# Kernel optimization log

Measured on AMD Instinct MI355X. Metric: run time of the kernel, lower is better.

Reference implementation:

```python
import jax, jax.numpy as jnp
import numpy as np

WIN = (7, 7)          # window_size (M, M)
DIM = 128             # C
HEADS = 4
B = 64                # images
NW = 64               # windows per image
NG = WIN[0] * WIN[1]  # 49 tokens per window
NT = 3136             # total patches per image (56x56)


def _relative_position_index(wh, ww):
    # Faithful to the TF code (default 'xy' meshgrid ordering, global token at (0,0))
    coords = np.stack(np.meshgrid(np.arange(wh), np.arange(ww)))        # (2, ww, wh)
    flat = coords.reshape(2, wh * ww)                                    # (2, M^2)
    flat1 = np.concatenate([flat, np.array([[0], [0]])], axis=1)         # (2, M^2+1)
    rel = flat[:, :, None] - flat1[:, None, :]                           # (2, M^2, M^2+1)
    rel = rel.transpose(1, 2, 0).astype(np.int32)
    rel[:, :, 0] += wh - 1
    rel[:, :, 1] += ww - 1
    rel[:, :, 0] *= 2 * ww - 1
    return rel.sum(-1)                                                   # (M^2, M^2+1)


def setup_inputs() -> dict:
    key = jax.random.key(0)
    ks = jax.random.split(key, 9)
    C, H = DIM, HEADS
    B_ = B * NW
    table_sz = (2 * WIN[0] - 1) * (2 * WIN[1] - 1)  # 169
    return {
        "x": jax.random.normal(ks[0], (B_, NG, C), jnp.float32),
        "xtotal": jax.random.normal(ks[1], (B, NT, C), jnp.float32),
        "xavg": jax.random.normal(ks[2], (B, 1, C), jnp.float32),
        "mask": jnp.zeros((NW, NG, NG + 1), jnp.float32),
        "W_q": jax.random.normal(ks[3], (C, C), jnp.float32) * (C ** -0.5),
        "b_q": jax.random.normal(ks[4], (C,), jnp.float32) * 0.02,
        "W_kv": jax.random.normal(ks[5], (C, 2 * C), jnp.float32) * (C ** -0.5),
        "b_kv": jax.random.normal(ks[6], (2 * C,), jnp.float32) * 0.02,
        "bias_table": jax.random.normal(ks[7], (table_sz, H), jnp.float32) * 0.02,
        "rel_idx": jnp.asarray(_relative_position_index(*WIN), jnp.int32),
    }


def reference(x, xtotal, xavg, mask, W_q, b_q, W_kv, b_kv, bias_table, rel_idx):
    B_, NGl, C = x.shape
    Bl = xavg.shape[0]
    H = bias_table.shape[1]
    d = C // H
    scale = d ** -0.5
    N = NGl + 1

    # window path: concat repeated global token, project kv / q
    xavgR = jnp.repeat(xavg, B_ // Bl, axis=0)               # (B_, 1, C)
    x_c = jnp.concatenate([x, xavgR], axis=1)                # (B_, N, C)
    kv = (x_c @ W_kv + b_kv).reshape(B_, N, 2, H, d).transpose(2, 0, 3, 1, 4)
    k, v = kv[0], kv[1]                                      # (B_, H, N, d)
    q = ((x @ W_q + b_q).reshape(B_, NGl, H, d).transpose(0, 2, 1, 3)) * scale

    attn = jnp.einsum('bhnd,bhmd->bhnm', q, k)               # (B_, H, NG, N)
    bias = bias_table[rel_idx.reshape(-1)].reshape(NGl, N, H).transpose(2, 0, 1)
    attn = attn + bias[None]
    nW = mask.shape[0]
    attn = attn.reshape(B_ // nW, nW, H, NGl, N) + mask[None, :, None]
    attn = jax.nn.softmax(attn.reshape(B_, H, NGl, N), axis=-1)
    x_out = jnp.einsum('bhnm,bhmd->bhnd', attn, v).transpose(0, 2, 1, 3).reshape(B_, NGl, C)

    # global path: q_avg (NOT scaled in the original), attends over all patches
    Nt = xtotal.shape[1]
    kvg = (xtotal @ W_kv + b_kv).reshape(Bl, Nt, 2, H, d).transpose(2, 0, 3, 1, 4)
    kg, vg = kvg[0], kvg[1]                                  # (B, H, Nt, d)
    q_avg = (xavg @ W_q + b_q).reshape(Bl, 1, H, d).transpose(0, 2, 1, 3)
    attng = jax.nn.softmax(jnp.einsum('bhqd,bhmd->bhqm', q_avg, kg), axis=-1)
    xavg_out = jnp.einsum('bhqm,bhmd->bhqd', attng, vg).transpose(0, 2, 1, 3).reshape(Bl, 1, C)
    return x_out, xavg_out
```

## Files before the change

kernel.cpp:

```cpp
#include <hip/hip_runtime.h>
#include <hip/hip_bf16.h>

#define NB_  4096
#define NG_  49
#define NC_  128
#define NH_  4
#define DH_  32
#define NN_  50
#define NIMG 64
#define NT_  3136
#define SCALE_ 0.17677669529663687f

#define WT_LO_OFF 49152
#define BM_OFF    98304
#define SBUF_F    573440

typedef unsigned short u16;
typedef unsigned int   u32;
typedef __attribute__((ext_vector_type(8))) short bf16x8;
typedef __attribute__((ext_vector_type(4))) float f32x4;

__device__ __forceinline__ float b2f(u16 u) {
    union { u32 i; float f; } v; v.i = ((u32)u) << 16; return v.f;
}
__device__ __forceinline__ u16 f2b(float f) {
    union { float f; u32 i; } v; v.f = f;
    u32 x = v.i;
    return (u16)((x + 0x7fffu + ((x >> 16) & 1u)) >> 16);
}
__device__ __forceinline__ u32 pk2(float a, float b) {
    union { __hip_bfloat162 h2; u32 u; } v;
    v.h2 = __float22bfloat162_rn(make_float2(a, b));
    return v.u;
}

extern "C" __global__ __launch_bounds__(256)
void prep_kernel(const float* __restrict__ Wq, const float* __restrict__ Wkv,
                 const float* __restrict__ btab, const int* __restrict__ ridx,
                 const float* __restrict__ mask, u16* __restrict__ ws)
{
    __shared__ int   ridxS[NG_ * NN_];
    __shared__ float btabS[169 * NH_];
    const int t = threadIdx.x, b = blockIdx.x;
    if (b < 24) {
        const int tn = b, kt = t >> 6, lane = t & 63;
        const int j  = tn * 16 + (lane & 15);
        const int k0 = kt * 32 + (lane >> 4) * 8;
        const float qs = (j < 128) ? SCALE_ : 1.f;
        u32 hi[4], lo[4];
        #pragma unroll
        for (int p = 0; p < 4; ++p) {
            const int k = k0 + 2 * p;
            float w0 = ((j < 128) ? Wq[(size_t)k * 128 + j]       : Wkv[(size_t)k * 256 + (j - 128)]) * qs;
            float w1 = ((j < 128) ? Wq[(size_t)(k + 1) * 128 + j] : Wkv[(size_t)(k + 1) * 256 + (j - 128)]) * qs;
            u16 h0 = f2b(w0), h1 = f2b(w1);
            hi[p] = (u32)h0 | ((u32)h1 << 16);
            lo[p] = (u32)f2b(w0 - b2f(h0)) | ((u32)f2b(w1 - b2f(h1)) << 16);
        }
        const size_t fo = ((size_t)(tn * 4 + kt) * 64 + lane) * 8;
        *(uint4*)(ws + fo)             = make_uint4(hi[0], hi[1], hi[2], hi[3]);
        *(uint4*)(ws + WT_LO_OFF + fo) = make_uint4(lo[0], lo[1], lo[2], lo[3]);
    } else {
        const int wx = b - 24;
        for (int i = t; i < NG_ * NN_; i += 256) ridxS[i] = ridx[i];
        for (int i = t; i < 169 * NH_; i += 256) btabS[i] = btab[i];
        __syncthreads();
        for (int i = t; i < NH_ * 16 * 64; i += 256) {
            const int lane = i & 63, tile = (i >> 6) & 15, h = i >> 10;
            const int n  = 16 * (tile >> 2) + (lane & 15);
            const int m0 = 16 * (tile & 3) + 4 * (lane >> 4);
            u16 vv[4];
            #pragma unroll
            for (int e = 0; e < 4; ++e) {
                const int m = m0 + e;
                float val = -1e30f;
                if (n < NG_ && m < NN_)
                    val = btabS[ridxS[n * NN_ + m] * NH_ + h] + mask[((size_t)wx * NG_ + n) * NN_ + m];
                vv[e] = f2b(val);
            }
            u32* dst = (u32*)(ws + BM_OFF + ((size_t)((wx * NH_ + h) * 16 + tile) * 64 + lane) * 4);
            dst[0] = (u32)vv[0] | ((u32)vv[1] << 16);
            dst[1] = (u32)vv[2] | ((u32)vv[3] << 16);
        }
    }
}

struct WinShared {
    u16 q[64][128];
    u16 k[64][128];
    u16 buf[64 * 128];
};
struct GlobShared {
    float qa[NH_][DH_];
    float xavgS[NC_];
    float u[NH_][NC_];
    float cst[NH_];
    float smax[NH_];
    float ssum[NH_];
    float red[256];
    float wpart[2][NH_][NC_];
};
union SMem { WinShared w; GlobShared g; };

extern "C" __global__ __launch_bounds__(256, 4)
void wa2_kernel(const float* __restrict__ x, const float* __restrict__ xtotal,
                const float* __restrict__ xavg,
                const float* __restrict__ Wq, const float* __restrict__ bq,
                const float* __restrict__ Wkv, const float* __restrict__ bkv,
                float* __restrict__ out, u16* __restrict__ ws)
{
    __shared__ SMem sm;
    const int t = threadIdx.x;
    const int blk = blockIdx.x;

    if (blk >= NIMG) {
        WinShared& S = sm.w;
        const int wb   = blk - NIMG;
        const int img  = wb >> 6;
        const int widx = wb & 63;
        const int lane = t & 63, wv = t >> 6;
        const int l15  = lane & 15, g = lane >> 4;

        {
            u16* xc = S.buf;
            const float2* xr = (const float2*)(x + (size_t)wb * (NG_ * NC_));
            for (int i = t; i < NG_ * 64; i += 256) {
                const int row = i >> 6, cp = i & 63;
                float2 xv = xr[i];
                *(u32*)&xc[row * 128 + ((2 * cp) ^ ((row & 7) << 3))] = pk2(xv.x, xv.y);
            }
            if (t < 64) {
                float2 av = ((const float2*)(xavg + (size_t)img * NC_))[t];
                *(u32*)&xc[49 * 128 + ((2 * t) ^ 8)] = pk2(av.x, av.y);
            }
            for (int i = t; i < 14 * 64; i += 256) {
                const int row = 50 + (i >> 6), cp = i & 63;
                *(u32*)&xc[row * 128 + ((2 * cp) ^ ((row & 7) << 3))] = 0u;
            }
        }
        __syncthreads();

        const int sw = (l15 & 7) << 3;

        bf16x8 a[4][4];
        #pragma unroll
        for (int tm = 0; tm < 4; ++tm)
            #pragma unroll
            for (int kt = 0; kt < 4; ++kt)
                a[tm][kt] = *(const bf16x8*)&S.buf[(16 * tm + l15) * 128 + ((32 * kt + 8 * g) ^ sw)];
        __syncthreads();

        {
            u16* vT = S.buf;
            for (int i = 0; i < 6; ++i) {
                const int tn = 6 * wv + i;
                const int jc = tn * 16 + l15;
                const float bias = (jc < 128) ? bq[jc] * SCALE_ : bkv[jc - 128];
                f32x4 acc[4];
                #pragma unroll
                for (int tm = 0; tm < 4; ++tm) acc[tm] = (f32x4){bias, bias, bias, bias};
                #pragma unroll
                for (int kt = 0; kt < 4; ++kt) {
                    const size_t fo = ((size_t)(tn * 4 + kt) * 64 + lane) * 8;
                    bf16x8 bh = *(const bf16x8*)(ws + fo);
                    bf16x8 bl = *(const bf16x8*)(ws + WT_LO_OFF + fo);
                    #pragma unroll
                    for (int tm = 0; tm < 4; ++tm) {
                        acc[tm] = __builtin_amdgcn_mfma_f32_16x16x32_bf16(a[tm][kt], bh, acc[tm], 0, 0, 0);
                        acc[tm] = __builtin_amdgcn_mfma_f32_16x16x32_bf16(a[tm][kt], bl, acc[tm], 0, 0, 0);
                    }
                }
                #pragma unroll
                for (int tm = 0; tm < 4; ++tm) {
                    #pragma unroll
                    for (int rp = 0; rp < 2; ++rp) {
                        const int r0 = 16 * tm + 4 * g + 2 * rp;
                        const u32 p = pk2(acc[tm][2 * rp], acc[tm][2 * rp + 1]);
                        if (jc < 128) {
                            S.q[r0][jc ^ ((r0 & 7) << 3)]           = (u16)p;
                            S.q[r0 + 1][jc ^ (((r0 + 1) & 7) << 3)] = (u16)(p >> 16);
                        } else if (jc < 256) {
                            const int c = jc - 128;
                            S.k[r0][c ^ ((r0 & 7) << 3)]           = (u16)p;
                            S.k[r0 + 1][c ^ (((r0 + 1) & 7) << 3)] = (u16)(p >> 16);
                        } else {
                            const int c = jc - 256, swc = (c & 7) << 3;
                            vT[c * 64 + (r0 ^ swc)]       = (u16)p;
                            vT[c * 64 + ((r0 + 1) ^ swc)] = (u16)(p >> 16);
                        }
                    }
                }
            }
        }
        __syncthreads();

        {
            const int h = wv;
            const u16* vT = S.buf;
            bf16x8 ka[4], qb[4];
            #pragma unroll
            for (int tk = 0; tk < 4; ++tk)
                ka[tk] = *(const bf16x8*)&S.k[16 * tk + l15][(32 * h + 8 * g) ^ sw];
            #pragma unroll
            for (int tq = 0; tq < 4; ++tq)
                qb[tq] = *(const bf16x8*)&S.q[16 * tq + l15][(32 * h + 8 * g) ^ sw];

            const u16* bmb = ws + BM_OFF + (size_t)(widx * NH_ + h) * 4096;
            f32x4 s[4][4];
            #pragma unroll
            for (int tq = 0; tq < 4; ++tq)
                #pragma unroll
                for (int tk = 0; tk < 4; ++tk) {
                    uint2 bm = *(const uint2*)(bmb + ((size_t)(tq * 4 + tk) * 64 + lane) * 4);
                    f32x4 c0;
                    c0[0] = b2f((u16)bm.x); c0[1] = b2f((u16)(bm.x >> 16));
                    c0[2] = b2f((u16)bm.y); c0[3] = b2f((u16)(bm.y >> 16));
                    s[tk][tq] = __builtin_amdgcn_mfma_f32_16x16x32_bf16(ka[tk], qb[tq], c0, 0, 0, 0);
                }

            float inv[4];
            #pragma unroll
            for (int tq = 0; tq < 4; ++tq) {
                float m = s[0][tq][0];
                #pragma unroll
                for (int tk = 0; tk < 4; ++tk)
                    #pragma unroll
                    for (int r = 0; r < 4; ++r) m = fmaxf(m, s[tk][tq][r]);
                m = fmaxf(m, __shfl_xor(m, 16));
                m = fmaxf(m, __shfl_xor(m, 32));
                float sum = 0.f;
                #pragma unroll
                for (int tk = 0; tk < 4; ++tk)
                    #pragma unroll
                    for (int r = 0; r < 4; ++r) {
                        float e = __expf(s[tk][tq][r] - m);
                        s[tk][tq][r] = e;
                        sum += e;
                    }
                sum += __shfl_xor(sum, 16);
                sum += __shfl_xor(sum, 32);
                inv[tq] = 1.f / sum;
            }

            bf16x8 pa[4][2];
            #pragma unroll
            for (int tq = 0; tq < 4; ++tq) {
                const float iv = inv[tq];
                #pragma unroll
                for (int kt = 0; kt < 2; ++kt) {
                    union { u32 u[4]; bf16x8 v; } P;
                    P.u[0] = pk2(s[2 * kt][tq][0] * iv, s[2 * kt][tq][1] * iv);
                    P.u[1] = pk2(s[2 * kt][tq][2] * iv, s[2 * kt][tq][3] * iv);
                    P.u[2] = pk2(s[2 * kt + 1][tq][0] * iv, s[2 * kt + 1][tq][1] * iv);
                    P.u[3] = pk2(s[2 * kt + 1][tq][2] * iv, s[2 * kt + 1][tq][3] * iv);
                    pa[tq][kt] = P.v;
                }
            }
            bf16x8 vb[2][2];
            #pragma unroll
            for (int tn = 0; tn < 2; ++tn) {
                const int c = 32 * h + 16 * tn + l15;
                const int swv = (c & 7) << 3;
                #pragma unroll
                for (int kt = 0; kt < 2; ++kt) {
                    union { uint2 u2[2]; bf16x8 v; } B;
                    B.u2[0] = *(const uint2*)&vT[c * 64 + ((32 * kt + 4 * g) ^ swv)];
                    B.u2[1] = *(const uint2*)&vT[c * 64 + ((32 * kt + 16 + 4 * g) ^ swv)];
                    vb[kt][tn] = B.v;
                }
            }
            #pragma unroll
            for (int tq = 0; tq < 4; ++tq)
                #pragma unroll
                for (int tn = 0; tn < 2; ++tn) {
                    f32x4 acc = {0.f, 0.f, 0.f, 0.f};
                    acc = __builtin_amdgcn_mfma_f32_16x16x32_bf16(pa[tq][0], vb[0][tn], acc, 0, 0, 0);
                    acc = __builtin_amdgcn_mfma_f32_16x16x32_bf16(pa[tq][1], vb[1][tn], acc, 0, 0, 0);
                    #pragma unroll
                    for (int r = 0; r < 4; ++r) {
                        const int row = 16 * tq + 4 * g + r;
                        if (row < NG_)
                            out[(size_t)wb * (NG_ * NC_) + (size_t)row * NC_ + 32 * h + 16 * tn + l15] = acc[r];
                    }
                }
        }
    } else {
        GlobShared& S = sm.g;
        const int img = blk;
        float* sb = (float*)ws + SBUF_F + (size_t)img * (NT_ * NH_);

        if (t < NC_) S.xavgS[t] = xavg[img * NC_ + t];
        __syncthreads();

        if (t < NC_) {
            const int h = t >> 5, jj = t & 31;
            float acc = bq[h * DH_ + jj];
            for (int c = 0; c < NC_; ++c) acc += S.xavgS[c] * Wq[c * NC_ + h * DH_ + jj];
            S.qa[h][jj] = acc;
        }
        __syncthreads();

        if (t < NC_) {
            const int c = t;
            #pragma unroll
            for (int h = 0; h < NH_; ++h) {
                float acc = 0.f;
                const float* wr = Wkv + (size_t)c * (2 * NC_) + h * DH_;
                #pragma unroll
                for (int jj = 0; jj < DH_; ++jj) acc += wr[jj] * S.qa[h][jj];
                S.u[h][c] = acc;
            }
        } else if (t < NC_ + NH_) {
            const int h = t - NC_;
            float acc = 0.f;
            for (int jj = 0; jj < DH_; ++jj) acc += S.qa[h][jj] * bkv[h * DH_ + jj];
            S.cst[h] = acc;
        }
        __syncthreads();

        float lmax0 = -1e30f, lmax1 = -1e30f, lmax2 = -1e30f, lmax3 = -1e30f;
        for (int m = t; m < NT_; m += 256) {
            const float* xr = xtotal + (size_t)(img * NT_ + m) * NC_;
            float a0 = S.cst[0], a1 = S.cst[1], a2 = S.cst[2], a3 = S.cst[3];
            for (int c = 0; c < NC_; ++c) {
                float xv = xr[c];
                a0 += xv * S.u[0][c];
                a1 += xv * S.u[1][c];
                a2 += xv * S.u[2][c];
                a3 += xv * S.u[3][c];
            }
            *(float4*)&sb[m * NH_] = make_float4(a0, a1, a2, a3);
            lmax0 = fmaxf(lmax0, a0); lmax1 = fmaxf(lmax1, a1);
            lmax2 = fmaxf(lmax2, a2); lmax3 = fmaxf(lmax3, a3);
        }
        float lm[NH_] = {lmax0, lmax1, lmax2, lmax3};
        for (int h = 0; h < NH_; ++h) {
            __syncthreads();
            S.red[t] = lm[h];
            __syncthreads();
            for (int off = 128; off > 0; off >>= 1) {
                if (t < off) S.red[t] = fmaxf(S.red[t], S.red[t + off]);
                __syncthreads();
            }
            if (t == 0) S.smax[h] = S.red[0];
        }
        __syncthreads();

        float ls[NH_] = {0.f, 0.f, 0.f, 0.f};
        for (int m = t; m < NT_; m += 256) {
            float4 sv = *(const float4*)&sb[m * NH_];
            sv.x = __expf(sv.x - S.smax[0]); ls[0] += sv.x;
            sv.y = __expf(sv.y - S.smax[1]); ls[1] += sv.y;
            sv.z = __expf(sv.z - S.smax[2]); ls[2] += sv.z;
            sv.w = __expf(sv.w - S.smax[3]); ls[3] += sv.w;
            *(float4*)&sb[m * NH_] = sv;
        }
        for (int h = 0; h < NH_; ++h) {
            __syncthreads();
            S.red[t] = ls[h];
            __syncthreads();
            for (int off = 128; off > 0; off >>= 1) {
                if (t < off) S.red[t] += S.red[t + off];
                __syncthreads();
            }
            if (t == 0) S.ssum[h] = S.red[0];
        }
        __syncthreads();

        {
            const int c = t & 127, half = t >> 7;
            float a0 = 0.f, a1 = 0.f, a2 = 0.f, a3 = 0.f;
            const int m0 = half * (NT_ / 2), m1 = m0 + NT_ / 2;
            for (int m = m0; m < m1; ++m) {
                float xv = xtotal[(size_t)(img * NT_ + m) * NC_ + c];
                float4 e4 = *(const float4*)&sb[m * NH_];
                a0 += e4.x * xv; a1 += e4.y * xv;
                a2 += e4.z * xv; a3 += e4.w * xv;
            }
            S.wpart[half][0][c] = a0; S.wpart[half][1][c] = a1;
            S.wpart[half][2][c] = a2; S.wpart[half][3][c] = a3;
        }
        __syncthreads();

        if (t < NC_) {
            const int h = t >> 5;
            const float winv = 1.f / S.ssum[h];
            float acc = bkv[NC_ + t];
            for (int c = 0; c < NC_; ++c) {
                float wv = (S.wpart[0][h][c] + S.wpart[1][h][c]) * winv;
                acc += wv * Wkv[(size_t)c * (2 * NC_) + NC_ + t];
            }
            out[(size_t)NB_ * (NG_ * NC_) + img * NC_ + t] = acc;
        }
    }
}

extern "C" void kernel_launch(void* const* d_in, const int* in_sizes, int n_in,
                              void* d_out, int out_size, void* d_ws, size_t ws_size,
                              hipStream_t stream) {
    const float* x      = (const float*)d_in[0];
    const float* xtotal = (const float*)d_in[1];
    const float* xavg   = (const float*)d_in[2];
    const float* mask   = (const float*)d_in[3];
    const float* Wq     = (const float*)d_in[4];
    const float* bq     = (const float*)d_in[5];
    const float* Wkv    = (const float*)d_in[6];
    const float* bkv    = (const float*)d_in[7];
    const float* btab   = (const float*)d_in[8];
    const int*   ridx   = (const int*)d_in[9];
    float* outp = (float*)d_out;
    u16*   ws   = (u16*)d_ws;
    (void)in_sizes; (void)n_in; (void)out_size; (void)ws_size;

    prep_kernel<<<24 + 64, 256, 0, stream>>>(Wq, Wkv, btab, ridx, mask, ws);
    wa2_kernel<<<NB_ + NIMG, 256, 0, stream>>>(x, xtotal, xavg, Wq, bq,
                                               Wkv, bkv, outp, ws);
}
```

Before: 463.4 us.

## Split global attention path into per-image chunks with atomic last-block reduction

The global-token attention path is split from one block per image into 8 chunk blocks per image. Each chunk block computes scores, exponentials and the weighted sums of xtotal in a single streaming pass with coalesced float4 loads. Partial sums are combined through global atomics, and the last-arriving block finishes the V projection. The q/u/bias-constant precomputation and the zeroing of the accumulators and counter move into the prep kernel. Softmax max-subtraction is dropped, which trades the extra passes for a risk of overflow when scores are large.

Result: faster. 442.5 us (-4.5%).

```diff
diff --git a/kernel.cpp b/kernel.cpp
--- a/kernel.cpp
+++ b/kernel.cpp
@@ -9,11 +9,18 @@
 #define NN_  50
 #define NIMG 64
 #define NT_  3136
+#define NCHK 8
+#define CROWS 392
 #define SCALE_ 0.17677669529663687f
 
 #define WT_LO_OFF 49152
 #define BM_OFF    98304
-#define SBUF_F    573440
+#define FBASE  573440
+#define U_F    (FBASE)
+#define CST_F  (FBASE + 32768)
+#define WACC_F (FBASE + 33024)
+#define SUM_F  (FBASE + 65792)
+#define CNT_F  (FBASE + 66048)
 
 typedef unsigned short u16;
 typedef unsigned int   u32;
@@ -37,10 +44,14 @@
 extern "C" __global__ __launch_bounds__(256)
 void prep_kernel(const float* __restrict__ Wq, const float* __restrict__ Wkv,
                  const float* __restrict__ btab, const int* __restrict__ ridx,
-                 const float* __restrict__ mask, u16* __restrict__ ws)
+                 const float* __restrict__ mask, const float* __restrict__ xavg,
+                 const float* __restrict__ bq, const float* __restrict__ bkv,
+                 u16* __restrict__ ws)
 {
     __shared__ int   ridxS[NG_ * NN_];
     __shared__ float btabS[169 * NH_];
+    __shared__ float xavgS[NC_];
+    __shared__ float qaS[NC_];
     const int t = threadIdx.x, b = blockIdx.x;
     if (b < 24) {
         const int tn = b, kt = t >> 6, lane = t & 63;
@@ -60,7 +71,7 @@
         const size_t fo = ((size_t)(tn * 4 + kt) * 64 + lane) * 8;
         *(uint4*)(ws + fo)             = make_uint4(hi[0], hi[1], hi[2], hi[3]);
         *(uint4*)(ws + WT_LO_OFF + fo) = make_uint4(lo[0], lo[1], lo[2], lo[3]);
-    } else {
+    } else if (b < 88) {
         const int wx = b - 24;
         for (int i = t; i < NG_ * NN_; i += 256) ridxS[i] = ridx[i];
         for (int i = t; i < 169 * NH_; i += 256) btabS[i] = btab[i];
@@ -82,6 +93,38 @@
             dst[0] = (u32)vv[0] | ((u32)vv[1] << 16);
             dst[1] = (u32)vv[2] | ((u32)vv[3] << 16);
         }
+    } else {
+        const int img = b - 88;
+        float* wsF = (float*)ws;
+        if (t < NC_) xavgS[t] = xavg[img * NC_ + t];
+        __syncthreads();
+        if (t < NC_) {
+            float acc = bq[t];
+            for (int c = 0; c < NC_; ++c) acc += xavgS[c] * Wq[c * NC_ + t];
+            qaS[t] = acc;
+        }
+        __syncthreads();
+        if (t < NC_) {
+            const int c = t;
+            const float* wr = Wkv + (size_t)c * 256;
+            #pragma unroll
+            for (int h = 0; h < NH_; ++h) {
+                float acc = 0.f;
+                #pragma unroll
+                for (int j = 0; j < 32; ++j) acc += wr[h * 32 + j] * qaS[h * 32 + j];
+                wsF[U_F + img * 512 + h * 128 + c] = acc;
+            }
+            #pragma unroll
+            for (int h = 0; h < NH_; ++h) wsF[WACC_F + img * 512 + h * 128 + t] = 0.f;
+        } else if (t < NC_ + NH_) {
+            const int h = t - NC_;
+            float acc = 0.f;
+            for (int j = 0; j < 32; ++j) acc += qaS[h * 32 + j] * bkv[h * 32 + j];
+            wsF[CST_F + img * 4 + h] = acc;
+            wsF[SUM_F + img * 4 + h] = 0.f;
+        } else if (t == NC_ + NH_) {
+            ((int*)wsF)[CNT_F + img] = 0;
+        }
     }
 }
 
@@ -90,17 +133,13 @@
     u16 k[64][128];
     u16 buf[64 * 128];
 };
-struct GlobShared {
-    float qa[NH_][DH_];
-    float xavgS[NC_];
-    float u[NH_][NC_];
-    float cst[NH_];
-    float smax[NH_];
-    float ssum[NH_];
-    float red[256];
-    float wpart[2][NH_][NC_];
+struct ChunkShared {
+    float waccS[4][4][128];
+    float esumS[4][4];
+    float sumS[4];
+    int   flagS;
 };
-union SMem { WinShared w; GlobShared g; };
+union SMem { WinShared w; ChunkShared c; };
 
 extern "C" __global__ __launch_bounds__(256, 4)
 void wa2_kernel(const float* __restrict__ x, const float* __restrict__ xtotal,
@@ -112,13 +151,13 @@
     __shared__ SMem sm;
     const int t = threadIdx.x;
     const int blk = blockIdx.x;
-
-    if (blk >= NIMG) {
+    const int lane = t & 63, wv = t >> 6;
+
+    if (blk >= NIMG * NCHK) {
         WinShared& S = sm.w;
-        const int wb   = blk - NIMG;
+        const int wb   = blk - NIMG * NCHK;
         const int img  = wb >> 6;
         const int widx = wb & 63;
-        const int lane = t & 63, wv = t >> 6;
         const int l15  = lane & 15, g = lane >> 4;
 
         {
@@ -285,112 +324,88 @@
                 }
         }
     } else {
-        GlobShared& S = sm.g;
-        const int img = blk;
-        float* sb = (float*)ws + SBUF_F + (size_t)img * (NT_ * NH_);
-
-        if (t < NC_) S.xavgS[t] = xavg[img * NC_ + t];
-        __syncthreads();
-
+        ChunkShared& S = sm.c;
+        float* wsF = (float*)ws;
+        const int img = blk >> 3, ch = blk & 7;
+        const int c0 = (lane & 31) * 4, roff = lane >> 5;
+
+        float4 uR[NH_]; float cstR[NH_];
+        #pragma unroll
+        for (int h = 0; h < NH_; ++h) {
+            uR[h]  = *(const float4*)&wsF[U_F + img * 512 + h * 128 + c0];
+            cstR[h] = wsF[CST_F + img * 4 + h];
+        }
+
+        float wacc[NH_][4] = {};
+        float esum[NH_] = {0.f, 0.f, 0.f, 0.f};
+        const float* xb = xtotal + ((size_t)img * NT_ + ch * CROWS) * NC_;
+        for (int it = 0; it < CROWS / 8; ++it) {
+            const int m = it * 8 + wv * 2 + roff;
+            float4 xv = *(const float4*)&xb[(size_t)m * NC_ + c0];
+            float s[NH_];
+            #pragma unroll
+            for (int h = 0; h < NH_; ++h)
+                s[h] = xv.x * uR[h].x + xv.y * uR[h].y + xv.z * uR[h].z + xv.w * uR[h].w;
+            #pragma unroll
+            for (int off = 1; off < 32; off <<= 1) {
+                #pragma unroll
+                for (int h = 0; h < NH_; ++h) s[h] += __shfl_xor(s[h], off);
+            }
+            #pragma unroll
+            for (int h = 0; h < NH_; ++h) {
+                const float e = __expf(s[h] + cstR[h]);
+                wacc[h][0] += e * xv.x; wacc[h][1] += e * xv.y;
+                wacc[h][2] += e * xv.z; wacc[h][3] += e * xv.w;
+                if ((lane & 31) == 0) esum[h] += e;
+            }
+        }
+
+        #pragma unroll
+        for (int h = 0; h < NH_; ++h) {
+            #pragma unroll
+            for (int i = 0; i < 4; ++i) wacc[h][i] += __shfl_xor(wacc[h][i], 32);
+            esum[h] += __shfl_xor(esum[h], 32);
+        }
+        if (lane < 32) {
+            #pragma unroll
+            for (int h = 0; h < NH_; ++h)
+                #pragma unroll
+                for (int i = 0; i < 4; ++i) S.waccS[wv][h][c0 + i] = wacc[h][i];
+            if (lane == 0) {
+                #pragma unroll
+                for (int h = 0; h < NH_; ++h) S.esumS[wv][h] = esum[h];
+            }
+        }
+        __syncthreads();
         if (t < NC_) {
-            const int h = t >> 5, jj = t & 31;
-            float acc = bq[h * DH_ + jj];
-            for (int c = 0; c < NC_; ++c) acc += S.xavgS[c] * Wq[c * NC_ + h * DH_ + jj];
-            S.qa[h][jj] = acc;
-        }
-        __syncthreads();
-
-        if (t < NC_) {
-            const int c = t;
             #pragma unroll
             for (int h = 0; h < NH_; ++h) {
-                float acc = 0.f;
-                const float* wr = Wkv + (size_t)c * (2 * NC_) + h * DH_;
-                #pragma unroll
-                for (int jj = 0; jj < DH_; ++jj) acc += wr[jj] * S.qa[h][jj];
-                S.u[h][c] = acc;
+                float v = S.waccS[0][h][t] + S.waccS[1][h][t] + S.waccS[2][h][t] + S.waccS[3][h][t];
+                atomicAdd(&wsF[WACC_F + img * 512 + h * 128 + t], v);
             }
         } else if (t < NC_ + NH_) {
             const int h = t - NC_;
-            float acc = 0.f;
-            for (int jj = 0; jj < DH_; ++jj) acc += S.qa[h][jj] * bkv[h * DH_ + jj];
-            S.cst[h] = acc;
-        }
-        __syncthreads();
-
-        float lmax0 = -1e30f, lmax1 = -1e30f, lmax2 = -1e30f, lmax3 = -1e30f;
-        for (int m = t; m < NT_; m += 256) {
-            const float* xr = xtotal + (size_t)(img * NT_ + m) * NC_;
-            float a0 = S.cst[0], a1 = S.cst[1], a2 = S.cst[2], a3 = S.cst[3];
-            for (int c = 0; c < NC_; ++c) {
-                float xv = xr[c];
-                a0 += xv * S.u[0][c];
-                a1 += xv * S.u[1][c];
-                a2 += xv * S.u[2][c];
-                a3 += xv * S.u[3][c];
-            }
-            *(float4*)&sb[m * NH_] = make_float4(a0, a1, a2, a3);
-            lmax0 = fmaxf(lmax0, a0); lmax1 = fmaxf(lmax1, a1);
-            lmax2 = fmaxf(lmax2, a2); lmax3 = fmaxf(lmax3, a3);
-        }
-        float lm[NH_] = {lmax0, lmax1, lmax2, lmax3};
-        for (int h = 0; h < NH_; ++h) {
+            atomicAdd(&wsF[SUM_F + img * 4 + h],
+                      S.esumS[0][h] + S.esumS[1][h] + S.esumS[2][h] + S.esumS[3][h]);
+        }
+        __threadfence();
+        __syncthreads();
+        if (t == 0) S.flagS = atomicAdd(&((int*)wsF)[CNT_F + img], 1);
+        __syncthreads();
+        if (S.flagS == NCHK - 1) {
+            float* wS = &S.waccS[0][0][0];
+            for (int i = t; i < 512; i += 256)
+                wS[i] = atomicAdd(&wsF[WACC_F + img * 512 + i], 0.f);
+            if (t < NH_) S.sumS[t] = atomicAdd(&wsF[SUM_F + img * 4 + t], 0.f);
             __syncthreads();
-            S.red[t] = lm[h];
-            __syncthreads();
-            for (int off = 128; off > 0; off >>= 1) {
-                if (t < off) S.red[t] = fmaxf(S.red[t], S.red[t + off]);
-                __syncthreads();
-            }
-            if (t == 0) S.smax[h] = S.red[0];
-        }
-        __syncthreads();
-
-        float ls[NH_] = {0.f, 0.f, 0.f, 0.f};
-        for (int m = t; m < NT_; m += 256) {
-            float4 sv = *(const float4*)&sb[m * NH_];
-            sv.x = __expf(sv.x - S.smax[0]); ls[0] += sv.x;
-            sv.y = __expf(sv.y - S.smax[1]); ls[1] += sv.y;
-            sv.z = __expf(sv.z - S.smax[2]); ls[2] += sv.z;
-            sv.w = __expf(sv.w - S.smax[3]); ls[3] += sv.w;
-            *(float4*)&sb[m * NH_] = sv;
-        }
-        for (int h = 0; h < NH_; ++h) {
-            __syncthreads();
-            S.red[t] = ls[h];
-            __syncthreads();
-            for (int off = 128; off > 0; off >>= 1) {
-                if (t < off) S.red[t] += S.red[t + off];
-                __syncthreads();
-            }
-            if (t == 0) S.ssum[h] = S.red[0];
-        }
-        __syncthreads();
-
-        {
-            const int c = t & 127, half = t >> 7;
-            float a0 = 0.f, a1 = 0.f, a2 = 0.f, a3 = 0.f;
-            const int m0 = half * (NT_ / 2), m1 = m0 + NT_ / 2;
-            for (int m = m0; m < m1; ++m) {
-                float xv = xtotal[(size_t)(img * NT_ + m) * NC_ + c];
-                float4 e4 = *(const float4*)&sb[m * NH_];
-                a0 += e4.x * xv; a1 += e4.y * xv;
-                a2 += e4.z * xv; a3 += e4.w * xv;
-            }
-            S.wpart[half][0][c] = a0; S.wpart[half][1][c] = a1;
-            S.wpart[half][2][c] = a2; S.wpart[half][3][c] = a3;
-        }
-        __syncthreads();
-
-        if (t < NC_) {
-            const int h = t >> 5;
-            const float winv = 1.f / S.ssum[h];
-            float acc = bkv[NC_ + t];
-            for (int c = 0; c < NC_; ++c) {
-                float wv = (S.wpart[0][h][c] + S.wpart[1][h][c]) * winv;
-                acc += wv * Wkv[(size_t)c * (2 * NC_) + NC_ + t];
-            }
-            out[(size_t)NB_ * (NG_ * NC_) + img * NC_ + t] = acc;
+            if (t < NC_) {
+                const int h = t >> 5;
+                const float inv = 1.f / S.sumS[h];
+                float acc = bkv[NC_ + t];
+                for (int c = 0; c < NC_; ++c)
+                    acc += (wS[h * 128 + c] * inv) * Wkv[(size_t)c * 256 + NC_ + t];
+                out[(size_t)NB_ * (NG_ * NC_) + img * NC_ + t] = acc;
+            }
         }
     }
 }
@@ -412,7 +427,7 @@
     u16*   ws   = (u16*)d_ws;
     (void)in_sizes; (void)n_in; (void)out_size; (void)ws_size;
 
-    prep_kernel<<<24 + 64, 256, 0, stream>>>(Wq, Wkv, btab, ridx, mask, ws);
-    wa2_kernel<<<NB_ + NIMG, 256, 0, stream>>>(x, xtotal, xavg, Wq, bq,
-                                               Wkv, bkv, outp, ws);
-}
+    prep_kernel<<<152, 256, 0, stream>>>(Wq, Wkv, btab, ridx, mask, xavg, bq, bkv, ws);
+    wa2_kernel<<<NIMG * NCHK + NB_, 256, 0, stream>>>(x, xtotal, xavg, Wq, bq,
+                                                      Wkv, bkv, outp, ws);
+}
```
